# Optimization experiments

Hardware: AMD Instinct MI355X
Metric: run time of the kernel (lower is better)

## Reference

```python
import jax, jax.numpy as jnp
import numpy as np

B, T, C, HS = 4, 2048, 2048, 64
H = C // HS
LW, LA, LV, LG = 64, 64, 32, 128
EPS_GN = 0.00064


def setup_inputs() -> dict:
    key = jax.random.key(0)
    ks = jax.random.split(key, 32)
    rn = lambda k, shape, s=1.0: jax.random.normal(k, shape, dtype=jnp.float32) * s
    return {
        "x": rn(ks[0], (B, T, C)),
        "v_first": rn(ks[1], (B, T, C)),
        "x_prev": rn(ks[2], (B, C)),
        "wkv_state": rn(ks[3], (B, H, HS, HS), 0.1),
        "x_r": rn(ks[4], (C,), 0.1),
        "x_w": rn(ks[5], (C,), 0.1),
        "x_k": rn(ks[6], (C,), 0.1),
        "x_v": rn(ks[7], (C,), 0.1),
        "x_a": rn(ks[8], (C,), 0.1),
        "x_g": rn(ks[9], (C,), 0.1),
        "w0": rn(ks[10], (C,), 0.1),
        "w1": rn(ks[11], (C, LW), 0.02),
        "w2": rn(ks[12], (LW, C), 0.02),
        "a0": rn(ks[13], (C,), 0.1),
        "a1": rn(ks[14], (C, LA), 0.02),
        "a2": rn(ks[15], (LA, C), 0.02),
        "v0": rn(ks[16], (C,), 0.1),
        "v1": rn(ks[17], (C, LV), 0.02),
        "v2": rn(ks[18], (LV, C), 0.02),
        "g1": rn(ks[19], (C, LG), 0.02),
        "g2": rn(ks[20], (LG, C), 0.02),
        "k_k": rn(ks[21], (C,), 0.1),
        "k_a": rn(ks[22], (C,), 0.1),
        "r_k": rn(ks[23], (H, HS), 0.1),
        "Wr": rn(ks[24], (C, C), 0.02),
        "Wk": rn(ks[25], (C, C), 0.02),
        "Wv": rn(ks[26], (C, C), 0.02),
        "Wo": rn(ks[27], (C, C), 0.02),
        "ln_w": jnp.ones((C,), dtype=jnp.float32),
        "ln_b": jnp.zeros((C,), dtype=jnp.float32),
    }


def _fwd(x, v_first, x_prev, wkv_state, x_r, x_w, x_k, x_v, x_a, x_g,
         w0, w1, w2, a0, a1, a2, v0, v1, v2, g1, g2, k_k, k_a, r_k,
         Wr, Wk, Wv, Wo, ln_w, ln_b):
    Bb, Tt, Cc = x.shape
    # token shift
    xx = jnp.concatenate([x_prev[:, None, :], x[:, :-1, :]], axis=1) - x
    xr = x + xx * x_r; xw = x + xx * x_w; xk = x + xx * x_k
    xv = x + xx * x_v; xa = x + xx * x_a; xg = x + xx * x_g
    r = xr @ Wr
    k = xk @ Wk
    v = xv @ Wv
    # log-decay: -softplus(-(w0 + tanh(xw@w1)@w2)) - 0.5  (<= -0.5)
    w_raw = -jax.nn.softplus(-(w0 + jnp.tanh(xw @ w1) @ w2)) - 0.5
    # layer_id != 0: mix with v_first
    v = v + (v_first - v) * jax.nn.sigmoid(v0 + (xv @ v1) @ v2)
    a = jax.nn.sigmoid(a0 + (xa @ a1) @ a2)
    g = jax.nn.sigmoid(xg @ g1) @ g2
    kk = (k * k_k).reshape(Bb, Tt, H, HS)
    kk = kk / jnp.maximum(jnp.linalg.norm(kk, axis=-1, keepdims=True), 1e-12)
    k = k * (1.0 + (a - 1.0) * k_a)
    rh = r.reshape(Bb, Tt, H, HS)
    kh = k.reshape(Bb, Tt, H, HS)
    vh = v.reshape(Bb, Tt, H, HS)
    ah = -kk                                  # removal direction
    bh = kk * a.reshape(Bb, Tt, H, HS)        # insertion direction
    wd = jnp.exp(-jnp.exp(w_raw)).reshape(Bb, Tt, H, HS)  # decay in (0,1)
    def step(st, ts):
        r_t, w_t, k_t, v_t, a_t, b_t = ts     # each [B,H,N]
        sa = jnp.einsum('bhij,bhj->bhi', st, a_t)
        st = st * w_t[:, :, None, :] + sa[..., None] * b_t[:, :, None, :] \
             + v_t[..., None] * k_t[:, :, None, :]
        return st, jnp.einsum('bhij,bhj->bhi', st, r_t)
    xs = tuple(jnp.moveaxis(t, 1, 0) for t in (rh, wd, kh, vh, ah, bh))
    _, out = jax.lax.scan(step, wkv_state, xs)
    out = jnp.moveaxis(out, 0, 1)             # [B,T,H,N]
    # GroupNorm(H groups) over each head's N channels
    mu = out.mean(-1, keepdims=True)
    var = out.var(-1, keepdims=True)
    out = ((out - mu) * jax.lax.rsqrt(var + EPS_GN)).reshape(Bb, Tt, Cc) * ln_w + ln_b
    bonus = (rh * kh * r_k).sum(-1, keepdims=True) * vh
    out = out + bonus.reshape(Bb, Tt, Cc)
    return (out * g) @ Wo


def reference(x, v_first, x_prev, wkv_state, x_r, x_w, x_k, x_v, x_a, x_g,
              w0, w1, w2, a0, a1, a2, v0, v1, v2, g1, g2, k_k, k_a, r_k,
              Wr, Wk, Wv, Wo, ln_w, ln_b):
    return _fwd(x, v_first, x_prev, wkv_state, x_r, x_w, x_k, x_v, x_a, x_g,
                w0, w1, w2, a0, a1, a2, v0, v1, v2, g1, g2, k_k, k_a, r_k,
                Wr, Wk, Wv, Wo, ln_w, ln_b)
```

## Files before the change

### kernel.cpp

```cpp
#include <hip/hip_runtime.h>

typedef float f32x4 __attribute__((ext_vector_type(4)));
typedef __bf16 bf16x8 __attribute__((ext_vector_type(8)));
typedef unsigned int u32x4 __attribute__((ext_vector_type(4)));

#define DI __device__ __forceinline__

constexpr int B_ = 4, T_ = 2048, C_ = 2048, H_ = 32;
constexpr int M_ = B_ * T_;

DI unsigned short f2bf(float f) {
  unsigned u = __float_as_uint(f);
  return (unsigned short)((u + 0x7FFFu + ((u >> 16) & 1u)) >> 16);
}
DI float bf2f(unsigned short h) { return __uint_as_float(((unsigned)h) << 16); }

DI void gl16(const void* g, void* l) {
  __builtin_amdgcn_global_load_lds(
      (__attribute__((address_space(1))) const unsigned int*)g,
      (__attribute__((address_space(3))) unsigned int*)l, 16, 0, 0);
}
DI void gl4(const void* g, void* l) {
  __builtin_amdgcn_global_load_lds(
      (__attribute__((address_space(1))) const unsigned int*)g,
      (__attribute__((address_space(3))) unsigned int*)l, 4, 0, 0);
}

DI float rsum8(float x) {
  int t = __builtin_amdgcn_update_dpp(0, __float_as_int(x), 0xB1, 0xF, 0xF, true);
  x += __int_as_float(t);
  t = __builtin_amdgcn_update_dpp(0, __float_as_int(x), 0x4E, 0xF, 0xF, true);
  x += __int_as_float(t);
  t = __builtin_amdgcn_update_dpp(0, __float_as_int(x), 0x141, 0xF, 0xF, true);
  x += __int_as_float(t);
  return x;
}

DI void tr_body(const float* __restrict__ in, unsigned short* __restrict__ out,
                int R, int C, int bx, int by, float (*tile)[33]) {
  int c0 = bx * 32, r0 = by * 32;
  int tx = threadIdx.x & 31, ty = threadIdx.x >> 5;
#pragma unroll
  for (int i = 0; i < 4; ++i) {
    int r = r0 + ty * 4 + i, c = c0 + tx;
    if (r < R && c < C) tile[ty * 4 + i][tx] = in[(size_t)r * C + c];
  }
  __syncthreads();
#pragma unroll
  for (int i = 0; i < 4; ++i) {
    int c = c0 + ty * 4 + i, r = r0 + tx;
    if (r < R && c < C) out[(size_t)c * R + r] = f2bf(tile[tx][ty * 4 + i]);
  }
}

__global__ __launch_bounds__(256) void k_transpose(const float* __restrict__ in,
                                                   unsigned short* __restrict__ out,
                                                   int R, int C) {
  __shared__ float tile[32][33];
  tr_body(in, out, R, C, blockIdx.x, blockIdx.y, tile);
}

__global__ __launch_bounds__(256) void k_transpose8(
    const float* w1, unsigned short* W1T, const float* a1, unsigned short* A1T,
    const float* v1, unsigned short* V1T, const float* g1, unsigned short* G1T,
    const float* w2, unsigned short* W2T, const float* a2, unsigned short* A2T,
    const float* v2, unsigned short* V2T, const float* g2, unsigned short* G2T) {
  __shared__ float tile[32][33];
  int b = blockIdx.x;
  if (b < 128)       tr_body(w1, W1T, 2048, 64, b % 2, b / 2, tile);
  else if (b < 256)  { b -= 128; tr_body(a1, A1T, 2048, 64, b % 2, b / 2, tile); }
  else if (b < 320)  { b -= 256; tr_body(v1, V1T, 2048, 32, 0, b, tile); }
  else if (b < 576)  { b -= 320; tr_body(g1, G1T, 2048, 128, b % 4, b / 4, tile); }
  else if (b < 704)  { b -= 576; tr_body(w2, W2T, 64, 2048, b % 64, b / 64, tile); }
  else if (b < 832)  { b -= 704; tr_body(a2, A2T, 64, 2048, b % 64, b / 64, tile); }
  else if (b < 896)  { b -= 832; tr_body(v2, V2T, 32, 2048, b % 64, b / 64, tile); }
  else               { b -= 896; tr_body(g2, G2T, 128, 2048, b % 64, b / 64, tile); }
}

DI void mix_emit(const float* coef, int c0, size_t off,
                 const float* xv, const float* dx, unsigned short* dst) {
  unsigned short u[8];
#pragma unroll
  for (int i = 0; i < 2; ++i) {
    f32x4 cf = *(const f32x4*)(coef + c0 + i * 4);
#pragma unroll
    for (int j = 0; j < 4; ++j) u[i * 4 + j] = f2bf(xv[i * 4 + j] + dx[i * 4 + j] * cf[j]);
  }
  u32x4 pv;
#pragma unroll
  for (int j = 0; j < 4; ++j) pv[j] = (unsigned)u[2 * j] | ((unsigned)u[2 * j + 1] << 16);
  *(u32x4*)(dst + off) = pv;
}

__global__ __launch_bounds__(256) void k_prep6(
    const float* __restrict__ x, const float* __restrict__ xprev,
    const float* __restrict__ cR, const float* __restrict__ cV,
    const float* __restrict__ cK, const float* __restrict__ cW,
    const float* __restrict__ cA, const float* __restrict__ cG,
    unsigned short* __restrict__ XR, unsigned short* __restrict__ XV,
    unsigned short* __restrict__ XK, unsigned short* __restrict__ XW,
    unsigned short* __restrict__ XA, unsigned short* __restrict__ XG) {
  int bt = blockIdx.x;
  int t = bt & (T_ - 1);
  int c0 = threadIdx.x * 8;
  size_t off = (size_t)bt * C_ + c0;
  const float* xp = x + off;
  const float* pp = t ? (xp - C_) : (xprev + (size_t)(bt >> 11) * C_ + c0);
  float xv[8], dx[8];
#pragma unroll
  for (int i = 0; i < 2; ++i) {
    f32x4 a = *(const f32x4*)(xp + i * 4);
    f32x4 p = *(const f32x4*)(pp + i * 4);
#pragma unroll
    for (int j = 0; j < 4; ++j) { xv[i * 4 + j] = a[j]; dx[i * 4 + j] = p[j] - a[j]; }
  }
  mix_emit(cR, c0, off, xv, dx, XR);
  mix_emit(cV, c0, off, xv, dx, XV);
  mix_emit(cK, c0, off, xv, dx, XK);
  mix_emit(cW, c0, off, xv, dx, XW);
  mix_emit(cA, c0, off, xv, dx, XA);
  mix_emit(cG, c0, off, xv, dx, XG);
}

template <int EPI>
__global__ __launch_bounds__(256, 2) void k_gemm_big(
    const unsigned short* __restrict__ A,
    const unsigned short* __restrict__ Bt,
    float* __restrict__ outF, unsigned short* __restrict__ outB,
    const unsigned short* __restrict__ svb, const float* __restrict__ vfirst,
    const unsigned short* __restrict__ abf,
    const float* __restrict__ k_k, const float* __restrict__ k_a,
    unsigned short* __restrict__ ahb, unsigned short* __restrict__ bhb) {
  __shared__ __align__(16) unsigned short As[128][64];
  __shared__ __align__(16) unsigned short Bs[128][64];
  const int tid = threadIdx.x, lane = tid & 63, wv = tid >> 6;
  const int bid = blockIdx.x;
  const int loc = bid >> 3;
  const int by = (bid & 7) * 8 + (loc & 7);
  const int bx = loc >> 3;
  const int m0 = by * 128, n0 = bx * 128;
  const int wm = (wv >> 1) * 64, wn = (wv & 1) * 64;
  const int lr = lane >> 3, lc = (lane & 7) * 8;
  f32x4 acc[4][4] = {};
  for (int kt = 0; kt < C_; kt += 64) {
    __syncthreads();
#pragma unroll
    for (int i = 0; i < 4; ++i) {
      int chunk = wv * 4 + i, r = chunk * 8 + lr;
      gl16(A + (size_t)(m0 + r) * C_ + kt + lc, (char*)&As[0][0] + chunk * 1024);
      gl16(Bt + (size_t)(n0 + r) * C_ + kt + lc, (char*)&Bs[0][0] + chunk * 1024);
    }
    __syncthreads();
    const int rr = lane & 15;
#pragma unroll
    for (int kh = 0; kh < 2; ++kh) {
      const int kof = kh * 32 + (lane >> 4) * 8;
      bf16x8 af[4], bfv[4];
#pragma unroll
      for (int i = 0; i < 4; ++i) af[i] = *(const bf16x8*)&As[wm + i * 16 + rr][kof];
#pragma unroll
      for (int j = 0; j < 4; ++j) bfv[j] = *(const bf16x8*)&Bs[wn + j * 16 + rr][kof];
#pragma unroll
      for (int i = 0; i < 4; ++i)
#pragma unroll
        for (int j = 0; j < 4; ++j)
          acc[i][j] = __builtin_amdgcn_mfma_f32_16x16x32_bf16(af[i], bfv[j], acc[i][j], 0, 0, 0);
    }
  }
  const int cr = (lane >> 4) * 4, cc2 = lane & 15;
  if constexpr (EPI == 2) {
    float kkv[4], kav[4];
#pragma unroll
    for (int j = 0; j < 4; ++j) {
      int col = n0 + wn + j * 16 + cc2;
      kkv[j] = k_k[col];
      kav[j] = k_a[col];
    }
#pragma unroll
    for (int i = 0; i < 4; ++i)
#pragma unroll
      for (int q = 0; q < 4; ++q) {
        int row = m0 + wm + i * 16 + cr + q;
        float kk4[4], p = 0.f;
#pragma unroll
        for (int j = 0; j < 4; ++j) {
          float kkc = acc[i][j][q] * kkv[j];
          kk4[j] = kkc;
          p += kkc * kkc;
        }
        p += __shfl_xor(p, 1); p += __shfl_xor(p, 2);
        p += __shfl_xor(p, 4); p += __shfl_xor(p, 8);
        float inv = 1.f / fmaxf(sqrtf(p), 1e-12f);
#pragma unroll
        for (int j = 0; j < 4; ++j) {
          int col = n0 + wn + j * 16 + cc2;
          size_t off = (size_t)row * C_ + col;
          float kkn = kk4[j] * inv;
          float a = bf2f(abf[off]);
          ahb[off] = f2bf(-kkn);
          bhb[off] = f2bf(kkn * a);
          outB[off] = f2bf(acc[i][j][q] * (1.f + (a - 1.f) * kav[j]));
        }
      }
  } else {
#pragma unroll
    for (int i = 0; i < 4; ++i)
#pragma unroll
      for (int j = 0; j < 4; ++j)
#pragma unroll
        for (int q = 0; q < 4; ++q) {
          int row = m0 + wm + i * 16 + cr + q;
          int col = n0 + wn + j * 16 + cc2;
          size_t off = (size_t)row * C_ + col;
          float v = acc[i][j][q];
          if constexpr (EPI == 0) {
            outB[off] = f2bf(v);
          } else if constexpr (EPI == 1) {
            float s = bf2f(svb[off]);
            outB[off] = f2bf(v + (vfirst[off] - v) * s);
          } else {
            outF[off] = v;
          }
        }
  }
}

template <int N, int ACT>
DI void down_body(int m0, unsigned short (*As)[64], unsigned short (*Bs)[64],
                  const unsigned short* __restrict__ A,
                  const unsigned short* __restrict__ Bt,
                  unsigned short* __restrict__ out) {
  const int tid = threadIdx.x, lane = tid & 63, wv = tid >> 6;
  const int wm = wv * 32;
  const int lr = lane >> 3, lc = (lane & 7) * 8;
  f32x4 acc[2][N / 16] = {};
  for (int kt = 0; kt < C_; kt += 64) {
    __syncthreads();
#pragma unroll
    for (int i = 0; i < 4; ++i) {
      int chunk = wv * 4 + i, r = chunk * 8 + lr;
      gl16(A + (size_t)(m0 + r) * C_ + kt + lc, (char*)&As[0][0] + chunk * 1024);
    }
#pragma unroll
    for (int i = 0; i < N / 32; ++i) {
      int chunk = wv * (N / 32) + i, r = chunk * 8 + lr;
      gl16(Bt + (size_t)r * C_ + kt + lc, (char*)&Bs[0][0] + chunk * 1024);
    }
    __syncthreads();
    const int rr = lane & 15;
#pragma unroll
    for (int kh = 0; kh < 2; ++kh) {
      const int kof = kh * 32 + (lane >> 4) * 8;
      bf16x8 af[2], bfv[N / 16];
#pragma unroll
      for (int i = 0; i < 2; ++i) af[i] = *(const bf16x8*)&As[wm + i * 16 + rr][kof];
#pragma unroll
      for (int j = 0; j < N / 16; ++j) bfv[j] = *(const bf16x8*)&Bs[j * 16 + rr][kof];
#pragma unroll
      for (int i = 0; i < 2; ++i)
#pragma unroll
        for (int j = 0; j < N / 16; ++j)
          acc[i][j] = __builtin_amdgcn_mfma_f32_16x16x32_bf16(af[i], bfv[j], acc[i][j], 0, 0, 0);
    }
  }
  const int cr = (lane >> 4) * 4, cc2 = lane & 15;
#pragma unroll
  for (int i = 0; i < 2; ++i)
#pragma unroll
    for (int j = 0; j < N / 16; ++j)
#pragma unroll
      for (int q = 0; q < 4; ++q) {
        int row = m0 + wm + i * 16 + cr + q;
        int col = j * 16 + cc2;
        float v = acc[i][j][q];
        if (ACT == 1) v = tanhf(v);
        else if (ACT == 2) v = 1.f / (1.f + expf(-v));
        out[(size_t)row * N + col] = f2bf(v);
      }
}

__global__ __launch_bounds__(256, 2) void k_down4(
    const unsigned short* __restrict__ XMw, const unsigned short* __restrict__ XMa,
    const unsigned short* __restrict__ XMv, const unsigned short* __restrict__ XMg,
    const unsigned short* __restrict__ W1T, const unsigned short* __restrict__ A1T,
    const unsigned short* __restrict__ V1T, const unsigned short* __restrict__ G1T,
    unsigned short* __restrict__ HWB, unsigned short* __restrict__ HAB,
    unsigned short* __restrict__ HVB, unsigned short* __restrict__ HGB) {
  __shared__ __align__(16) unsigned short As[128][64];
  __shared__ __align__(16) unsigned short Bs[128][64];
  int g = blockIdx.x >> 6;
  int m0 = (blockIdx.x & 63) * 128;
  if (g == 0)      down_body<64, 1>(m0, As, Bs, XMw, W1T, HWB);
  else if (g == 1) down_body<64, 0>(m0, As, Bs, XMa, A1T, HAB);
  else if (g == 2) down_body<32, 0>(m0, As, Bs, XMv, V1T, HVB);
  else             down_body<128, 2>(m0, As, Bs, XMg, G1T, HGB);
}

template <int K, int MODE>
__global__ __launch_bounds__(256, 2) void k_up(
    const unsigned short* __restrict__ A, const unsigned short* __restrict__ Bt,
    const float* __restrict__ bias, float* __restrict__ outF,
    unsigned short* __restrict__ outB) {
  __shared__ __align__(16) unsigned short As[128][K];
  __shared__ __align__(16) unsigned short Bs[128][K];
  const int tid = threadIdx.x, lane = tid & 63, wv = tid >> 6;
  const int m0 = blockIdx.y * 128, n0 = blockIdx.x * 128;
  const int wm = (wv >> 1) * 64, wn = (wv & 1) * 64;
  constexpr int LPR = K / 8;
  constexpr int RPC = 64 / LPR;
  const int lr = lane / LPR, lc = (lane % LPR) * 8;
  f32x4 acc[4][4] = {};
#pragma unroll
  for (int i = 0; i < K / 16; ++i) {
    int chunk = wv * (K / 16) + i;
    int r = chunk * RPC + lr;
    gl16(A + (size_t)(m0 + r) * K + lc, (char*)&As[0][0] + chunk * 1024);
    gl16(Bt + (size_t)(n0 + r) * K + lc, (char*)&Bs[0][0] + chunk * 1024);
  }
  __syncthreads();
  const int rr = lane & 15;
#pragma unroll
  for (int ks = 0; ks < K / 32; ++ks) {
    const int kof = ks * 32 + (lane >> 4) * 8;
    bf16x8 af[4], bfv[4];
#pragma unroll
    for (int i = 0; i < 4; ++i) af[i] = *(const bf16x8*)&As[wm + i * 16 + rr][kof];
#pragma unroll
    for (int j = 0; j < 4; ++j) bfv[j] = *(const bf16x8*)&Bs[wn + j * 16 + rr][kof];
#pragma unroll
    for (int i = 0; i < 4; ++i)
#pragma unroll
      for (int j = 0; j < 4; ++j)
        acc[i][j] = __builtin_amdgcn_mfma_f32_16x16x32_bf16(af[i], bfv[j], acc[i][j], 0, 0, 0);
  }
  const int cr = (lane >> 4) * 4, cc2 = lane & 15;
#pragma unroll
  for (int i = 0; i < 4; ++i)
#pragma unroll
    for (int j = 0; j < 4; ++j)
#pragma unroll
      for (int q = 0; q < 4; ++q) {
        int row = m0 + wm + i * 16 + cr + q;
        int col = n0 + wn + j * 16 + cc2;
        size_t off = (size_t)row * C_ + col;
        float up = acc[i][j][q];
        if (MODE == 0) {
          float z = -(bias[col] + up);
          float sp = fmaxf(z, 0.f) + log1pf(expf(-fabsf(z)));
          outF[off] = expf(-expf(-sp - 0.5f));
        } else if (MODE == 1) {
          outB[off] = f2bf(1.f / (1.f + expf(-(bias[col] + up))));
        } else {
          outB[off] = f2bf(up);
        }
      }
}

__global__ __launch_bounds__(64) void k_scan(
    const unsigned short* __restrict__ RB, const float* __restrict__ WD,
    const unsigned short* __restrict__ KB, const unsigned short* __restrict__ VB,
    const unsigned short* __restrict__ AHB, const unsigned short* __restrict__ BHB,
    const float* __restrict__ s0, float* __restrict__ out) {
  __shared__ __align__(16) char sl[8][1024];
  const int lane = threadIdx.x & 63;
  const int p = blockIdx.x;
  const int wr = p >> 7, bh = p & 127;
  const int b = bh >> 5, h = bh & 31;
  const int e = lane & 7, rl = lane >> 3;
  const int row = wr * 8 + rl;
  const int e16 = e * 16;
  const size_t base = (size_t)b * T_ * C_ + h * 64;
  float S[8];
  {
    const float* sp = s0 + ((size_t)(b * H_ + h) * 64 + row) * 64 + e * 8;
    f32x4 s0v = *(const f32x4*)sp, s1v = *(const f32x4*)(sp + 4);
#pragma unroll
    for (int j = 0; j < 4; ++j) { S[j] = s0v[j]; S[4 + j] = s1v[j]; }
  }

#define ISSUE(t, slot)                                                        \
  {                                                                           \
    int ti = (t) < T_ ? (t) : T_ - 1;                                         \
    size_t eo = base + (size_t)ti * C_;                                       \
    char* d = &sl[slot][0];                                                   \
    const char* s1 = lane < 32 ? (const char*)(RB + eo) + lane * 4            \
                               : (const char*)(KB + eo) + (lane - 32) * 4;    \
    gl4(s1, d);                                                               \
    const char* s2 = lane < 32 ? (const char*)(AHB + eo) + lane * 4           \
                               : (const char*)(BHB + eo) + (lane - 32) * 4;   \
    gl4(s2, d + 256);                                                         \
    gl4((const char*)(WD + eo) + lane * 4, d + 512);                          \
    gl4((const char*)(VB + eo) + lane * 4, d + 768);                          \
  }

#define STEP(t, slot)                                                         \
  {                                                                           \
    asm volatile("s_waitcnt vmcnt(16)" ::: "memory");                         \
    __builtin_amdgcn_sched_barrier(0);                                        \
    const char* bp = &sl[slot][0];                                            \
    bf16x8 rv8 = *(const bf16x8*)(bp + e16);                                  \
    bf16x8 kv8 = *(const bf16x8*)(bp + 128 + e16);                            \
    bf16x8 av8 = *(const bf16x8*)(bp + 256 + e16);                            \
    bf16x8 bv8 = *(const bf16x8*)(bp + 384 + e16);                            \
    f32x4 w0 = *(const f32x4*)(bp + 512 + e * 32);                            \
    f32x4 w1 = *(const f32x4*)(bp + 528 + e * 32);                            \
    float vi = bf2f(*(const unsigned short*)(bp + 768 + row * 2));            \
    float rr[8], kk[8], aa[8], bv[8], ww[8];                                  \
    _Pragma("unroll") for (int j = 0; j < 8; ++j) {                           \
      rr[j] = (float)rv8[j];                                                  \
      kk[j] = (float)kv8[j];                                                  \
      aa[j] = (float)av8[j];                                                  \
      bv[j] = (float)bv8[j];                                                  \
    }                                                                         \
    _Pragma("unroll") for (int j = 0; j < 4; ++j) {                           \
      ww[j] = w0[j];                                                          \
      ww[4 + j] = w1[j];                                                      \
    }                                                                         \
    float sa0 = S[0] * aa[0], sa1 = S[1] * aa[1];                             \
    _Pragma("unroll") for (int j = 2; j < 8; j += 2) {                        \
      sa0 = fmaf(S[j], aa[j], sa0);                                           \
      sa1 = fmaf(S[j + 1], aa[j + 1], sa1);                                   \
    }                                                                         \
    float sa = rsum8(sa0 + sa1);                                              \
    float o0 = 0.f, o1 = 0.f;                                                 \
    _Pragma("unroll") for (int j = 0; j < 8; j += 2) {                        \
      S[j] = fmaf(S[j], ww[j], fmaf(sa, bv[j], vi * kk[j]));                  \
      S[j + 1] = fmaf(S[j + 1], ww[j + 1],                                    \
                      fmaf(sa, bv[j + 1], vi * kk[j + 1]));                   \
      o0 = fmaf(S[j], rr[j], o0);                                             \
      o1 = fmaf(S[j + 1], rr[j + 1], o1);                                     \
    }                                                                         \
    float o = rsum8(o0 + o1);                                                 \
    if (e == 0) out[base + (size_t)(t) * C_ + row] = o;                       \
  }

  ISSUE(0, 0) ISSUE(1, 1) ISSUE(2, 2) ISSUE(3, 3)
#pragma unroll 1
  for (int t = 0; t < T_; t += 8) {
    ISSUE(t + 4, 4)  STEP(t + 0, 0)
    ISSUE(t + 5, 5)  STEP(t + 1, 1)
    ISSUE(t + 6, 6)  STEP(t + 2, 2)
    ISSUE(t + 7, 7)  STEP(t + 3, 3)
    ISSUE(t + 8, 0)  STEP(t + 4, 4)
    ISSUE(t + 9, 1)  STEP(t + 5, 5)
    ISSUE(t + 10, 2) STEP(t + 6, 6)
    ISSUE(t + 11, 3) STEP(t + 7, 7)
  }
#undef ISSUE
#undef STEP
}

__global__ __launch_bounds__(256) void k_gn(
    const float* __restrict__ o, const unsigned short* __restrict__ rb,
    const unsigned short* __restrict__ kb, const unsigned short* __restrict__ v,
    const unsigned short* __restrict__ g, const float* __restrict__ r_k,
    const float* __restrict__ lnw, const float* __restrict__ lnb,
    unsigned short* __restrict__ outg) {
  int wid = blockIdx.x * 4 + (threadIdx.x >> 6);
  int lane = threadIdx.x & 63;
  int h = wid & (H_ - 1);
  size_t bt = (size_t)(wid >> 5);
  size_t off = bt * C_ + h * 64 + lane;
  int c = h * 64 + lane;
  float x = o[off];
  float mu = x;
#pragma unroll
  for (int m = 1; m < 64; m <<= 1) mu += __shfl_xor(mu, m);
  mu *= (1.f / 64.f);
  float d = x - mu;
  float var = d * d;
#pragma unroll
  for (int m = 1; m < 64; m <<= 1) var += __shfl_xor(var, m);
  var *= (1.f / 64.f);
  float y = d * rsqrtf(var + 6.4e-4f) * lnw[c] + lnb[c];
  float bd = bf2f(rb[off]) * bf2f(kb[off]) * r_k[c];
#pragma unroll
  for (int m = 1; m < 64; m <<= 1) bd += __shfl_xor(bd, m);
  float res = (y + bd * bf2f(v[off])) * bf2f(g[off]);
  outg[off] = f2bf(res);
}

extern "C" void kernel_launch(void* const* d_in, const int* in_sizes, int n_in,
                              void* d_out, int out_size, void* d_ws, size_t ws_size,
                              hipStream_t stream) {
  const float* x      = (const float*)d_in[0];
  const float* vfirst = (const float*)d_in[1];
  const float* xprev  = (const float*)d_in[2];
  const float* wkv0   = (const float*)d_in[3];
  const float* x_r = (const float*)d_in[4];
  const float* x_w = (const float*)d_in[5];
  const float* x_k = (const float*)d_in[6];
  const float* x_v = (const float*)d_in[7];
  const float* x_a = (const float*)d_in[8];
  const float* x_g = (const float*)d_in[9];
  const float* w0 = (const float*)d_in[10];
  const float* w1 = (const float*)d_in[11];
  const float* w2 = (const float*)d_in[12];
  const float* a0 = (const float*)d_in[13];
  const float* a1 = (const float*)d_in[14];
  const float* a2 = (const float*)d_in[15];
  const float* v0 = (const float*)d_in[16];
  const float* v1 = (const float*)d_in[17];
  const float* v2 = (const float*)d_in[18];
  const float* g1 = (const float*)d_in[19];
  const float* g2 = (const float*)d_in[20];
  const float* k_k = (const float*)d_in[21];
  const float* k_a = (const float*)d_in[22];
  const float* r_k = (const float*)d_in[23];
  const float* Wr = (const float*)d_in[24];
  const float* Wk = (const float*)d_in[25];
  const float* Wv = (const float*)d_in[26];
  const float* Wo = (const float*)d_in[27];
  const float* lnw = (const float*)d_in[28];
  const float* lnb = (const float*)d_in[29];
  float* out = (float*)d_out;
  char* ws = (char*)d_ws;

  size_t woff = 0;
  auto alloc = [&](size_t n) { char* p = ws + woff; woff += n; return p; };
  char* R1 = alloc(67108864);
  unsigned short* ABF = (unsigned short*)R1;
  unsigned short* SVB = (unsigned short*)(R1 + 33554432);
  float* WD = (float*)R1;
  unsigned short* WT  = (unsigned short*)alloc(8388608);
  unsigned short* W1T = (unsigned short*)alloc(262144);
  unsigned short* A1T = (unsigned short*)alloc(262144);
  unsigned short* V1T = (unsigned short*)alloc(131072);
  unsigned short* G1T = (unsigned short*)alloc(524288);
  unsigned short* W2T = (unsigned short*)alloc(262144);
  unsigned short* A2T = (unsigned short*)alloc(262144);
  unsigned short* V2T = (unsigned short*)alloc(131072);
  unsigned short* G2T = (unsigned short*)alloc(524288);
  unsigned short* HWB = (unsigned short*)alloc(1048576);
  unsigned short* HAB = (unsigned short*)alloc(1048576);
  unsigned short* HVB = (unsigned short*)alloc(524288);
  unsigned short* HGB = (unsigned short*)alloc(2097152);
  unsigned short* RB  = (unsigned short*)alloc(33554432);
  unsigned short* KB  = (unsigned short*)alloc(33554432);
  unsigned short* VB  = (unsigned short*)alloc(33554432);
  unsigned short* AHB = (unsigned short*)alloc(33554432);
  unsigned short* BHB = (unsigned short*)alloc(33554432);
  alloc(65536);
  unsigned short* XMr = VB;
  unsigned short* XMv = KB;
  unsigned short* XMk = (unsigned short*)out;
  unsigned short* XMw = AHB;
  unsigned short* XMa = BHB;
  unsigned short* XMg = RB;
  unsigned short* GBF  = AHB;
  unsigned short* OUTG = BHB;

  dim3 blk(256);
  dim3 gg(16, 64);
  dim3 g1d(1024);

  k_transpose8<<<dim3(1152), blk, 0, stream>>>(w1, W1T, a1, A1T, v1, V1T, g1, G1T,
                                               w2, W2T, a2, A2T, v2, V2T, g2, G2T);

  k_prep6<<<dim3(M_), blk, 0, stream>>>(x, xprev, x_r, x_v, x_k, x_w, x_a, x_g,
                                        XMr, XMv, XMk, XMw, XMa, XMg);

  k_down4<<<dim3(256), blk, 0, stream>>>(XMw, XMa, XMv, XMg,
                                         W1T, A1T, V1T, G1T, HWB, HAB, HVB, HGB);

  k_up<64, 1><<<gg, blk, 0, stream>>>(HAB, A2T, a0, nullptr, ABF);
  k_up<32, 1><<<gg, blk, 0, stream>>>(HVB, V2T, v0, nullptr, SVB);

  k_transpose<<<dim3(64, 64), blk, 0, stream>>>(Wr, WT, 2048, 2048);
  k_gemm_big<0><<<g1d, blk, 0, stream>>>(XMr, WT,
      nullptr, RB, nullptr, nullptr, nullptr, nullptr, nullptr, nullptr, nullptr);

  k_transpose<<<dim3(64, 64), blk, 0, stream>>>(Wv, WT, 2048, 2048);
  k_gemm_big<1><<<g1d, blk, 0, stream>>>(XMv, WT,
      nullptr, VB, SVB, vfirst, nullptr, nullptr, nullptr, nullptr, nullptr);

  k_transpose<<<dim3(64, 64), blk, 0, stream>>>(Wk, WT, 2048, 2048);
  k_gemm_big<2><<<g1d, blk, 0, stream>>>(XMk, WT,
      nullptr, KB, nullptr, nullptr, ABF, k_k, k_a, AHB, BHB);

  k_up<64, 0><<<gg, blk, 0, stream>>>(HWB, W2T, w0, WD, nullptr);

  k_scan<<<dim3(1024), dim3(64), 0, stream>>>(RB, WD, KB, VB, AHB, BHB, wkv0, out);

  k_up<128, 3><<<gg, blk, 0, stream>>>(HGB, G2T, nullptr, nullptr, GBF);

  k_gn<<<dim3(65536), blk, 0, stream>>>(out, RB, KB, VB, GBF, r_k, lnw, lnb, OUTG);

  k_transpose<<<dim3(64, 64), blk, 0, stream>>>(Wo, WT, 2048, 2048);
  k_gemm_big<3><<<g1d, blk, 0, stream>>>(OUTG, WT,
      out, nullptr, nullptr, nullptr, nullptr, nullptr, nullptr, nullptr, nullptr);
}
```

Measured before the change: 1.458 ms.

## Split WKV scan state across 16 lanes per row, doubling scan blocks

Each scan wave now handles 4 state rows, with each of 16 lanes holding 4 state elements, instead of 8 rows with 8 elements per lane. The grid doubles to 2048 single-wave blocks, which shortens the per-step serial FMA chain and raises parallelism for the latency-bound recurrence. The cost is twice the global-to-LDS load traffic, since each block reloads the full per-timestep r/k/a/b/w/v vectors for fewer rows. Each step also needs a longer DPP reduction across 16 lanes.

```diff
diff --git a/kernel.cpp b/kernel.cpp
--- a/kernel.cpp
+++ b/kernel.cpp
@@ -2,6 +2,7 @@
 
 typedef float f32x4 __attribute__((ext_vector_type(4)));
 typedef __bf16 bf16x8 __attribute__((ext_vector_type(8)));
+typedef __bf16 bf16x4 __attribute__((ext_vector_type(4)));
 typedef unsigned int u32x4 __attribute__((ext_vector_type(4)));
 
 #define DI __device__ __forceinline__
@@ -26,12 +27,14 @@
       (__attribute__((address_space(3))) unsigned int*)l, 4, 0, 0);
 }
 
-DI float rsum8(float x) {
+DI float rsum16(float x) {
   int t = __builtin_amdgcn_update_dpp(0, __float_as_int(x), 0xB1, 0xF, 0xF, true);
   x += __int_as_float(t);
   t = __builtin_amdgcn_update_dpp(0, __float_as_int(x), 0x4E, 0xF, 0xF, true);
   x += __int_as_float(t);
-  t = __builtin_amdgcn_update_dpp(0, __float_as_int(x), 0x141, 0xF, 0xF, true);
+  t = __builtin_amdgcn_update_dpp(0, __float_as_int(x), 0x124, 0xF, 0xF, true);
+  x += __int_as_float(t);
+  t = __builtin_amdgcn_update_dpp(0, __float_as_int(x), 0x128, 0xF, 0xF, true);
   x += __int_as_float(t);
   return x;
 }
@@ -364,19 +367,12 @@
   __shared__ __align__(16) char sl[8][1024];
   const int lane = threadIdx.x & 63;
   const int p = blockIdx.x;
-  const int wr = p >> 7, bh = p & 127;
+  const int wq = p >> 7, bh = p & 127;
   const int b = bh >> 5, h = bh & 31;
-  const int e = lane & 7, rl = lane >> 3;
-  const int row = wr * 8 + rl;
-  const int e16 = e * 16;
+  const int e = lane & 15, rl = lane >> 4;
+  const int row = wq * 4 + rl;
   const size_t base = (size_t)b * T_ * C_ + h * 64;
-  float S[8];
-  {
-    const float* sp = s0 + ((size_t)(b * H_ + h) * 64 + row) * 64 + e * 8;
-    f32x4 s0v = *(const f32x4*)sp, s1v = *(const f32x4*)(sp + 4);
-#pragma unroll
-    for (int j = 0; j < 4; ++j) { S[j] = s0v[j]; S[4 + j] = s1v[j]; }
-  }
+  f32x4 S = *(const f32x4*)(s0 + ((size_t)(b * H_ + h) * 64 + row) * 64 + e * 4);
 
 #define ISSUE(t, slot)                                                        \
   {                                                                           \
@@ -398,39 +394,30 @@
     asm volatile("s_waitcnt vmcnt(16)" ::: "memory");                         \
     __builtin_amdgcn_sched_barrier(0);                                        \
     const char* bp = &sl[slot][0];                                            \
-    bf16x8 rv8 = *(const bf16x8*)(bp + e16);                                  \
-    bf16x8 kv8 = *(const bf16x8*)(bp + 128 + e16);                            \
-    bf16x8 av8 = *(const bf16x8*)(bp + 256 + e16);                            \
-    bf16x8 bv8 = *(const bf16x8*)(bp + 384 + e16);                            \
-    f32x4 w0 = *(const f32x4*)(bp + 512 + e * 32);                            \
-    f32x4 w1 = *(const f32x4*)(bp + 528 + e * 32);                            \
+    bf16x4 rv = *(const bf16x4*)(bp + e * 8);                                 \
+    bf16x4 kv = *(const bf16x4*)(bp + 128 + e * 8);                           \
+    bf16x4 av = *(const bf16x4*)(bp + 256 + e * 8);                           \
+    bf16x4 bv4 = *(const bf16x4*)(bp + 384 + e * 8);                          \
+    f32x4 wv = *(const f32x4*)(bp + 512 + e * 16);                            \
     float vi = bf2f(*(const unsigned short*)(bp + 768 + row * 2));            \
-    float rr[8], kk[8], aa[8], bv[8], ww[8];                                  \
-    _Pragma("unroll") for (int j = 0; j < 8; ++j) {                           \
-      rr[j] = (float)rv8[j];                                                  \
-      kk[j] = (float)kv8[j];                                                  \
-      aa[j] = (float)av8[j];                                                  \
-      bv[j] = (float)bv8[j];                                                  \
+    float rr[4], kk[4], aa[4], bb[4];                                         \
+    _Pragma("unroll") for (int j = 0; j < 4; ++j) {                           \
+      rr[j] = (float)rv[j];                                                   \
+      kk[j] = (float)kv[j];                                                   \
+      aa[j] = (float)av[j];                                                   \
+      bb[j] = (float)bv4[j];                                                  \
     }                                                                         \
+    float sa = S[0] * aa[0];                                                  \
+    sa = fmaf(S[1], aa[1], sa);                                               \
+    sa = fmaf(S[2], aa[2], sa);                                               \
+    sa = fmaf(S[3], aa[3], sa);                                               \
+    sa = rsum16(sa);                                                          \
+    float o = 0.f;                                                            \
     _Pragma("unroll") for (int j = 0; j < 4; ++j) {                           \
-      ww[j] = w0[j];                                                          \
-      ww[4 + j] = w1[j];                                                      \
+      S[j] = fmaf(S[j], wv[j], fmaf(sa, bb[j], vi * kk[j]));                  \
+      o = fmaf(S[j], rr[j], o);                                               \
     }                                                                         \
-    float sa0 = S[0] * aa[0], sa1 = S[1] * aa[1];                             \
-    _Pragma("unroll") for (int j = 2; j < 8; j += 2) {                        \
-      sa0 = fmaf(S[j], aa[j], sa0);                                           \
-      sa1 = fmaf(S[j + 1], aa[j + 1], sa1);                                   \
-    }                                                                         \
-    float sa = rsum8(sa0 + sa1);                                              \
-    float o0 = 0.f, o1 = 0.f;                                                 \
-    _Pragma("unroll") for (int j = 0; j < 8; j += 2) {                        \
-      S[j] = fmaf(S[j], ww[j], fmaf(sa, bv[j], vi * kk[j]));                  \
-      S[j + 1] = fmaf(S[j + 1], ww[j + 1],                                    \
-                      fmaf(sa, bv[j + 1], vi * kk[j + 1]));                   \
-      o0 = fmaf(S[j], rr[j], o0);                                             \
-      o1 = fmaf(S[j + 1], rr[j + 1], o1);                                     \
-    }                                                                         \
-    float o = rsum8(o0 + o1);                                                 \
+    o = rsum16(o);                                                            \
     if (e == 0) out[base + (size_t)(t) * C_ + row] = o;                       \
   }
 
@@ -580,7 +567,7 @@
 
   k_up<64, 0><<<gg, blk, 0, stream>>>(HWB, W2T, w0, WD, nullptr);
 
-  k_scan<<<dim3(1024), dim3(64), 0, stream>>>(RB, WD, KB, VB, AHB, BHB, wkv0, out);
+  k_scan<<<dim3(2048), dim3(64), 0, stream>>>(RB, WD, KB, VB, AHB, BHB, wkv0, out);
 
   k_up<128, 3><<<gg, blk, 0, stream>>>(HGB, G2T, nullptr, nullptr, GBF);
 
```

After: 1.411 ms. 1.03x faster.
